# Kernel optimization log

Measured on AMD Instinct MI355X. Metric: run time of the kernel, lower is better.

Reference implementation:

```python
import jax, jax.numpy as jnp
import numpy as np

N = 100000   # nodes
E = 1600000  # edges
G = 256      # graphs
NF = 7       # node features
EF = 3       # edge features (in/out)
UD = 2       # global feature dim
H = 128      # hidden dim
NL = 2       # MetaLayers = n_layers - 1
DOUT = 1


def _lin_init(k, fan_in, fan_out):
    return jax.random.normal(k, (fan_in, fan_out), jnp.float32) / np.sqrt(fan_in)


def _mlp2(h, W1, b1, W2, b2):
    return jax.nn.relu(h @ W1 + b1) @ W2 + b2


def setup_inputs() -> dict:
    key = jax.random.key(0)
    ks = jax.random.split(key, 40)
    x = jax.random.normal(ks[0], (N, NF), jnp.float32)
    edge_index = jax.random.randint(ks[1], (2, E), 0, N, jnp.int64)
    edge_attr = jax.random.normal(ks[2], (E, EF), jnp.float32)
    u = jax.random.normal(ks[3], (G, UD), jnp.float32)
    batch = jnp.sort(jax.random.randint(ks[4], (N,), 0, G, jnp.int64))
    # stacked per-layer params (NL identical layers)
    e_in = 2 * NF + EF          # 17
    n_in = NF + 3 * EF + UD     # 18
    eW1 = jnp.stack([_lin_init(ks[5 + i], e_in, H) for i in range(NL)])
    eb1 = jnp.zeros((NL, H), jnp.float32)
    eW2 = jnp.stack([_lin_init(ks[7 + i], H, EF) for i in range(NL)])
    eb2 = jnp.zeros((NL, EF), jnp.float32)
    nW1 = jnp.stack([_lin_init(ks[9 + i], n_in, H) for i in range(NL)])
    nb1 = jnp.zeros((NL, H), jnp.float32)
    nW2 = jnp.stack([_lin_init(ks[11 + i], H, NF) for i in range(NL)])
    nb2 = jnp.zeros((NL, NF), jnp.float32)
    # output head: 3*node_out + global_in -> H -> H -> H -> dim_out
    oW1 = _lin_init(ks[20], 3 * NF + UD, H); ob1 = jnp.zeros((H,), jnp.float32)
    oW2 = _lin_init(ks[21], H, H); ob2 = jnp.zeros((H,), jnp.float32)
    oW3 = _lin_init(ks[22], H, H); ob3 = jnp.zeros((H,), jnp.float32)
    oW4 = _lin_init(ks[23], H, DOUT); ob4 = jnp.zeros((DOUT,), jnp.float32)
    return dict(x=x, edge_attr=edge_attr, u=u,
                eW1=eW1, eb1=eb1, eW2=eW2, eb2=eb2,
                nW1=nW1, nb1=nb1, nW2=nW2, nb2=nb2,
                oW1=oW1, ob1=ob1, oW2=oW2, ob2=ob2,
                oW3=oW3, ob3=ob3, oW4=oW4, ob4=ob4,
                edge_index=edge_index, batch=batch)


def _segment_reduce3(vals, seg, num):
    # add / max (empty -> 0, matching torch_scatter fill) / mean
    s = jax.ops.segment_sum(vals, seg, num_segments=num)
    cnt = jax.ops.segment_sum(jnp.ones((vals.shape[0], 1), vals.dtype), seg, num_segments=num)
    m = jax.ops.segment_max(vals, seg, num_segments=num)
    m = jnp.where(cnt > 0, m, jnp.zeros_like(m))
    mean = s / jnp.maximum(cnt, 1.0)
    return s, m, mean, cnt


def reference(x, edge_attr, u, eW1, eb1, eW2, eb2, nW1, nb1, nW2, nb2,
              oW1, ob1, oW2, ob2, oW3, ob3, oW4, ob4, edge_index, batch):
    row, col = edge_index[0], edge_index[1]
    for l in range(NL):
        # EdgeModel: gather src/dest node feats + edge feats -> MLP
        e_in = jnp.concatenate([x[row], x[col], edge_attr], axis=1)  # [E, 2*NF+EF]
        edge_attr = _mlp2(e_in, eW1[l], eb1[l], eW2[l], eb2[l])      # [E, EF]
        # NodeModel: three scatter reductions over incoming edges (col)
        s, m, mean, _ = _segment_reduce3(edge_attr, col, N)
        n_in = jnp.concatenate([x, s, m, mean, u[batch]], axis=1)    # [N, NF+3*EF+UD]
        x = _mlp2(n_in, nW1[l], nb1[l], nW2[l], nb2[l])              # [N, NF]
    # global pools per graph
    s, m, mean, _ = _segment_reduce3(x, batch, G)
    h = jnp.concatenate([s, mean, m, u], axis=1)                     # [G, 3*NF+UD]
    h = jax.nn.relu(h @ oW1 + ob1)
    h = jax.nn.relu(h @ oW2 + ob2)
    h = jax.nn.relu(h @ oW3 + ob3)
    return h @ oW4 + ob4                                             # [G, DOUT]
```

## Files before the change

### kernel.cpp

```cpp
#include <hip/hip_runtime.h>

#define NN 100000
#define NE 1600000
#define NG 256
#define NB 391

__global__ __launch_bounds__(256) void zero_kernel(float* __restrict__ p, int n) {
    int i = blockIdx.x * 256 + threadIdx.x;
    if (i < n) p[i] = 0.f;
}

__global__ __launch_bounds__(256) void rank_kernel(
    const int* __restrict__ col, unsigned* __restrict__ cnt,
    unsigned* __restrict__ rank) {
    int e = blockIdx.x * 256 + threadIdx.x;
    rank[e] = atomicAdd(&cnt[col[e]], 1u);
}

__global__ __launch_bounds__(256) void gbound_kernel(
    const int* __restrict__ batch, int* __restrict__ gstart) {
    int n = blockIdx.x * 256 + threadIdx.x;
    if (n >= NN) return;
    int b = batch[n];
    int bp = (n == 0) ? -1 : batch[n - 1];
    for (int g = bp + 1; g <= b; ++g) gstart[g] = n;
    if (n == NN - 1) {
        for (int g = b + 1; g <= NG; ++g) gstart[g] = NN;
    }
}

__global__ __launch_bounds__(256) void bsum_kernel(
    const unsigned* __restrict__ cnt, unsigned* __restrict__ bsum) {
    __shared__ unsigned sm[256];
    int i = blockIdx.x * 256 + threadIdx.x;
    sm[threadIdx.x] = (i < NN) ? cnt[i] : 0u;
    __syncthreads();
    for (int s = 128; s > 0; s >>= 1) {
        if (threadIdx.x < s) sm[threadIdx.x] += sm[threadIdx.x + s];
        __syncthreads();
    }
    if (threadIdx.x == 0) bsum[blockIdx.x] = sm[0];
}

__global__ __launch_bounds__(512) void bscan_kernel(
    const unsigned* __restrict__ bsum, unsigned* __restrict__ boff) {
    __shared__ unsigned a[512], b[512];
    int t = threadIdx.x;
    a[t] = (t < NB) ? bsum[t] : 0u;
    __syncthreads();
    unsigned* src = a; unsigned* dst = b;
    for (int off = 1; off < 512; off <<= 1) {
        unsigned v = src[t];
        if (t >= off) v += src[t - off];
        dst[t] = v;
        __syncthreads();
        unsigned* tmp = src; src = dst; dst = tmp;
    }
    if (t < NB) boff[t] = (t == 0) ? 0u : src[t - 1];
}

__global__ __launch_bounds__(256) void start_kernel(
    const unsigned* __restrict__ cnt, const unsigned* __restrict__ boff,
    unsigned* __restrict__ start) {
    __shared__ unsigned a[256], b[256];
    int t = threadIdx.x;
    int i = blockIdx.x * 256 + t;
    unsigned v = (i < NN) ? cnt[i] : 0u;
    a[t] = v;
    __syncthreads();
    unsigned* src = a; unsigned* dst = b;
    for (int off = 1; off < 256; off <<= 1) {
        unsigned x = src[t];
        if (t >= off) x += src[t - off];
        dst[t] = x;
        __syncthreads();
        unsigned* tmp = src; src = dst; dst = tmp;
    }
    unsigned excl = src[t] - v;
    unsigned st = boff[blockIdx.x] + excl;
    if (i < NN) {
        start[i] = st;
        if (i == NN - 1) start[NN] = st + v;
    }
}

__global__ __launch_bounds__(256) void scatter_kernel(
    const int* __restrict__ row, const int* __restrict__ col,
    const float* __restrict__ ea,
    const unsigned* __restrict__ start, const unsigned* __restrict__ rank,
    int2* __restrict__ rc, float* __restrict__ eab) {
    int e = blockIdx.x * 256 + threadIdx.x;
    int c = col[e];
    unsigned t = start[c] + rank[e];
    rc[t] = make_int2(row[e], c);
    eab[(size_t)t * 3 + 0] = ea[(size_t)e * 3 + 0];
    eab[(size_t)t * 3 + 1] = ea[(size_t)e * 3 + 1];
    eab[(size_t)t * 3 + 2] = ea[(size_t)e * 3 + 2];
}

__global__ __launch_bounds__(256) void prep_kernel(
    const float* __restrict__ eW1, const float* __restrict__ eb1, const float* __restrict__ eW2,
    const float* __restrict__ nW1, const float* __restrict__ nb1, const float* __restrict__ nW2,
    float* __restrict__ ewt, float* __restrict__ nwt)
{
    int t = blockIdx.x * 256 + threadIdx.x;
    const int ESZ = 2 * 128 * 24;
    const int NSZ = 2 * 128 * 28;
    if (t < ESZ) {
        int l = t / (128 * 24), rest = t % (128 * 24), j = rest / 24, i = rest % 24;
        float v = 0.f;
        if (i < 17)       v = eW1[l * 17 * 128 + i * 128 + j];
        else if (i == 17) v = eb1[l * 128 + j];
        else if (i < 21)  v = eW2[l * 128 * 3 + j * 3 + (i - 18)];
        ewt[t] = v;
    } else if (t < ESZ + NSZ) {
        int q = t - ESZ;
        int l = q / (128 * 28), rest = q % (128 * 28), j = rest / 28, i = rest % 28;
        float v = 0.f;
        if (i < 18)       v = nW1[l * 18 * 128 + i * 128 + j];
        else if (i == 18) v = nb1[l * 128 + j];
        else if (i < 26)  v = nW2[l * 128 * 7 + j * 7 + (i - 19)];
        nwt[q] = v;
    }
}

__global__ __launch_bounds__(256) void edge_kernel(
    const float* __restrict__ x, float* eab,
    const int2* __restrict__ rc,
    const float* __restrict__ wt, const float* __restrict__ b2)
{
    int base = blockIdx.x * 1024 + threadIdx.x;
    int tt[4];
    bool ok[4];
    float in[4][17];

    #pragma unroll
    for (int k = 0; k < 4; ++k) {
        int t = base + k * 256;
        ok[k] = (t < NE);
        tt[k] = ok[k] ? t : 0;
        int2 p = rc[tt[k]];
        const float* xr = x + (size_t)p.x * 7;
        const float* xc = x + (size_t)p.y * 7;
        #pragma unroll
        for (int i = 0; i < 7; ++i) in[k][i] = xr[i];
        #pragma unroll
        for (int i = 0; i < 7; ++i) in[k][7 + i] = xc[i];
        #pragma unroll
        for (int i = 0; i < 3; ++i) in[k][14 + i] = eab[(size_t)tt[k] * 3 + i];
    }

    asm volatile("" : "+v"(in[0][0]), "+v"(in[0][1]), "+v"(in[0][2]), "+v"(in[0][3]),
                      "+v"(in[0][4]), "+v"(in[0][5]), "+v"(in[0][6]), "+v"(in[0][7]),
                      "+v"(in[0][8]), "+v"(in[0][9]), "+v"(in[0][10]), "+v"(in[0][11]),
                      "+v"(in[0][12]), "+v"(in[0][13]), "+v"(in[0][14]), "+v"(in[0][15]),
                      "+v"(in[0][16]));
    asm volatile("" : "+v"(in[1][0]), "+v"(in[1][1]), "+v"(in[1][2]), "+v"(in[1][3]),
                      "+v"(in[1][4]), "+v"(in[1][5]), "+v"(in[1][6]), "+v"(in[1][7]),
                      "+v"(in[1][8]), "+v"(in[1][9]), "+v"(in[1][10]), "+v"(in[1][11]),
                      "+v"(in[1][12]), "+v"(in[1][13]), "+v"(in[1][14]), "+v"(in[1][15]),
                      "+v"(in[1][16]));
    asm volatile("" : "+v"(in[2][0]), "+v"(in[2][1]), "+v"(in[2][2]), "+v"(in[2][3]),
                      "+v"(in[2][4]), "+v"(in[2][5]), "+v"(in[2][6]), "+v"(in[2][7]),
                      "+v"(in[2][8]), "+v"(in[2][9]), "+v"(in[2][10]), "+v"(in[2][11]),
                      "+v"(in[2][12]), "+v"(in[2][13]), "+v"(in[2][14]), "+v"(in[2][15]),
                      "+v"(in[2][16]));
    asm volatile("" : "+v"(in[3][0]), "+v"(in[3][1]), "+v"(in[3][2]), "+v"(in[3][3]),
                      "+v"(in[3][4]), "+v"(in[3][5]), "+v"(in[3][6]), "+v"(in[3][7]),
                      "+v"(in[3][8]), "+v"(in[3][9]), "+v"(in[3][10]), "+v"(in[3][11]),
                      "+v"(in[3][12]), "+v"(in[3][13]), "+v"(in[3][14]), "+v"(in[3][15]),
                      "+v"(in[3][16]));

    float acc[4][3];
    #pragma unroll
    for (int k = 0; k < 4; ++k) { acc[k][0] = 0.f; acc[k][1] = 0.f; acc[k][2] = 0.f; }

    #pragma unroll 4
    for (int j = 0; j < 128; ++j) {
        const float* wr = wt + __builtin_amdgcn_readfirstlane(j * 24);
        float w[21];
        #pragma unroll
        for (int i = 0; i < 21; ++i) w[i] = wr[i];
        float h0[4], h1[4];
        #pragma unroll
        for (int k = 0; k < 4; ++k) { h0[k] = w[17]; h1[k] = 0.f; }
        #pragma unroll
        for (int k = 0; k < 4; ++k) {
            h0[k] += in[k][0] * w[0];   h1[k] += in[k][1] * w[1];
            h0[k] += in[k][2] * w[2];   h1[k] += in[k][3] * w[3];
            h0[k] += in[k][4] * w[4];   h1[k] += in[k][5] * w[5];
            h0[k] += in[k][6] * w[6];   h1[k] += in[k][7] * w[7];
            h0[k] += in[k][8] * w[8];   h1[k] += in[k][9] * w[9];
            h0[k] += in[k][10] * w[10]; h1[k] += in[k][11] * w[11];
            h0[k] += in[k][12] * w[12]; h1[k] += in[k][13] * w[13];
            h0[k] += in[k][14] * w[14]; h1[k] += in[k][15] * w[15];
            h0[k] += in[k][16] * w[16];
        }
        #pragma unroll
        for (int k = 0; k < 4; ++k) {
            float h = fmaxf(h0[k] + h1[k], 0.f);
            acc[k][0] += h * w[18];
            acc[k][1] += h * w[19];
            acc[k][2] += h * w[20];
        }
    }

    float bb0 = b2[0], bb1 = b2[1], bb2 = b2[2];
    #pragma unroll
    for (int k = 0; k < 4; ++k) {
        if (ok[k]) {
            eab[(size_t)tt[k] * 3 + 0] = acc[k][0] + bb0;
            eab[(size_t)tt[k] * 3 + 1] = acc[k][1] + bb1;
            eab[(size_t)tt[k] * 3 + 2] = acc[k][2] + bb2;
        }
    }
}

__global__ __launch_bounds__(256) void reduce_kernel(
    const float* __restrict__ eab, const unsigned* __restrict__ start,
    const float* __restrict__ u, const int* __restrict__ batch,
    float* __restrict__ nred)
{
    int gid = blockIdx.x * 256 + threadIdx.x;
    int n = gid >> 4, sub = gid & 15;
    if (n >= NN) return;
    unsigned sbeg = start[n], send = start[n + 1];

    float s0 = 0.f, s1 = 0.f, s2 = 0.f;
    float m0 = -__builtin_inff(), m1 = -__builtin_inff(), m2 = -__builtin_inff();
    for (unsigned k = sbeg + sub; k < send; k += 16) {
        float v0 = eab[(size_t)k * 3 + 0];
        float v1 = eab[(size_t)k * 3 + 1];
        float v2 = eab[(size_t)k * 3 + 2];
        s0 += v0; s1 += v1; s2 += v2;
        m0 = fmaxf(m0, v0); m1 = fmaxf(m1, v1); m2 = fmaxf(m2, v2);
    }
    #pragma unroll
    for (int msk = 1; msk < 16; msk <<= 1) {
        s0 += __shfl_xor(s0, msk, 16);
        s1 += __shfl_xor(s1, msk, 16);
        s2 += __shfl_xor(s2, msk, 16);
        m0 = fmaxf(m0, __shfl_xor(m0, msk, 16));
        m1 = fmaxf(m1, __shfl_xor(m1, msk, 16));
        m2 = fmaxf(m2, __shfl_xor(m2, msk, 16));
    }
    if (sub == 0) {
        float deg = (float)(send - sbeg);
        if (send == sbeg) { m0 = 0.f; m1 = 0.f; m2 = 0.f; }
        float inv = 1.f / fmaxf(deg, 1.f);
        int b = batch[n];
        float* o = nred + (size_t)n * 12;
        o[0] = s0; o[1] = s1; o[2] = s2;
        o[3] = m0; o[4] = m1; o[5] = m2;
        o[6] = s0 * inv; o[7] = s1 * inv; o[8] = s2 * inv;
        o[9] = u[b * 2 + 0]; o[10] = u[b * 2 + 1];
    }
}

#define NMLP_BLOCKS 1024
#define NMLP_WAVES (NMLP_BLOCKS * 4)
__global__ __launch_bounds__(256, 4) void nodemlp_kernel(
    const float* x_in, const float* __restrict__ nred,
    const float* __restrict__ wt, const float* __restrict__ b2,
    float* x_out)
{
    int lane = threadIdx.x & 63;
    int wid = (blockIdx.x * 256 + threadIdx.x) >> 6;

    const float* ra = wt + lane * 28;
    const float* rb = wt + (lane + 64) * 28;
    float a0 = ra[0], a1 = ra[1], a2 = ra[2], a3 = ra[3], a4 = ra[4], a5 = ra[5],
          a6 = ra[6], a7 = ra[7], a8 = ra[8], a9 = ra[9], a10 = ra[10], a11 = ra[11],
          a12 = ra[12], a13 = ra[13], a14 = ra[14], a15 = ra[15], a16 = ra[16], a17 = ra[17],
          ab = ra[18], p0 = ra[19], p1 = ra[20], p2 = ra[21], p3 = ra[22], p4 = ra[23],
          p5 = ra[24], p6 = ra[25];
    float b0 = rb[0], b1 = rb[1], b2_ = rb[2], b3 = rb[3], b4 = rb[4], b5 = rb[5],
          b6 = rb[6], b7 = rb[7], b8 = rb[8], b9 = rb[9], b10 = rb[10], b11 = rb[11],
          b12 = rb[12], b13 = rb[13], b14 = rb[14], b15 = rb[15], b16 = rb[16], b17 = rb[17],
          bb = rb[18], q0 = rb[19], q1 = rb[20], q2 = rb[21], q3 = rb[22], q4 = rb[23],
          q5 = rb[24], q6 = rb[25];

    asm volatile("" : "+v"(a0), "+v"(a1), "+v"(a2), "+v"(a3), "+v"(a4), "+v"(a5),
                      "+v"(a6), "+v"(a7), "+v"(a8), "+v"(a9), "+v"(a10), "+v"(a11),
                      "+v"(a12), "+v"(a13), "+v"(a14), "+v"(a15), "+v"(a16), "+v"(a17),
                      "+v"(ab), "+v"(p0), "+v"(p1), "+v"(p2), "+v"(p3), "+v"(p4),
                      "+v"(p5), "+v"(p6));
    asm volatile("" : "+v"(b0), "+v"(b1), "+v"(b2_), "+v"(b3), "+v"(b4), "+v"(b5),
                      "+v"(b6), "+v"(b7), "+v"(b8), "+v"(b9), "+v"(b10), "+v"(b11),
                      "+v"(b12), "+v"(b13), "+v"(b14), "+v"(b15), "+v"(b16), "+v"(b17),
                      "+v"(bb), "+v"(q0), "+v"(q1), "+v"(q2), "+v"(q3), "+v"(q4),
                      "+v"(q5), "+v"(q6));

    float B0 = b2[0], B1 = b2[1], B2 = b2[2], B3 = b2[3], B4 = b2[4], B5 = b2[5], B6 = b2[6];

    const int nper = (NN + NMLP_WAVES - 1) / NMLP_WAVES;
    int n0 = wid * nper;
    int n1 = n0 + nper; if (n1 > NN) n1 = NN;

    #pragma unroll 2
    for (int n = n0; n < n1; ++n) {
        int nu = __builtin_amdgcn_readfirstlane(n);
        const float* xp = x_in + (size_t)nu * 7;
        const float* rp = nred + (size_t)nu * 12;
        float i0 = xp[0], i1 = xp[1], i2 = xp[2], i3 = xp[3], i4 = xp[4], i5 = xp[5], i6 = xp[6];
        float s0 = rp[0], s1 = rp[1], s2 = rp[2];
        float m0 = rp[3], m1 = rp[4], m2 = rp[5];
        float e0 = rp[6], e1 = rp[7], e2 = rp[8];
        float u0 = rp[9], u1 = rp[10];

        float ha = ab, hb = bb;
        ha += i0 * a0;  hb += i0 * b0;
        ha += i1 * a1;  hb += i1 * b1;
        ha += i2 * a2;  hb += i2 * b2_;
        ha += i3 * a3;  hb += i3 * b3;
        ha += i4 * a4;  hb += i4 * b4;
        ha += i5 * a5;  hb += i5 * b5;
        ha += i6 * a6;  hb += i6 * b6;
        ha += s0 * a7;  hb += s0 * b7;
        ha += s1 * a8;  hb += s1 * b8;
        ha += s2 * a9;  hb += s2 * b9;
        ha += m0 * a10; hb += m0 * b10;
        ha += m1 * a11; hb += m1 * b11;
        ha += m2 * a12; hb += m2 * b12;
        ha += e0 * a13; hb += e0 * b13;
        ha += e1 * a14; hb += e1 * b14;
        ha += e2 * a15; hb += e2 * b15;
        ha += u0 * a16; hb += u0 * b16;
        ha += u1 * a17; hb += u1 * b17;
        ha = fmaxf(ha, 0.f); hb = fmaxf(hb, 0.f);

        float c0 = ha * p0 + hb * q0;
        float c1 = ha * p1 + hb * q1;
        float c2 = ha * p2 + hb * q2;
        float c3 = ha * p3 + hb * q3;
        float c4 = ha * p4 + hb * q4;
        float c5 = ha * p5 + hb * q5;
        float c6 = ha * p6 + hb * q6;
        #pragma unroll
        for (int msk = 1; msk < 64; msk <<= 1) {
            c0 += __shfl_xor(c0, msk);
            c1 += __shfl_xor(c1, msk);
            c2 += __shfl_xor(c2, msk);
            c3 += __shfl_xor(c3, msk);
            c4 += __shfl_xor(c4, msk);
            c5 += __shfl_xor(c5, msk);
            c6 += __shfl_xor(c6, msk);
        }
        float o = c0 + B0;
        if (lane == 1) o = c1 + B1;
        if (lane == 2) o = c2 + B2;
        if (lane == 3) o = c3 + B3;
        if (lane == 4) o = c4 + B4;
        if (lane == 5) o = c5 + B5;
        if (lane == 6) o = c6 + B6;
        if (lane < 7) x_out[(size_t)nu * 7 + lane] = o;
    }
}

__global__ __launch_bounds__(256) void pool_head_kernel(
    const float* __restrict__ x, const int* __restrict__ gstart,
    const float* __restrict__ u,
    const float* __restrict__ oW1, const float* __restrict__ ob1,
    const float* __restrict__ oW2, const float* __restrict__ ob2,
    const float* __restrict__ oW3, const float* __restrict__ ob3,
    const float* __restrict__ oW4, const float* __restrict__ ob4,
    float* __restrict__ out)
{
    int g = blockIdx.x, tid = threadIdx.x;
    int lane = tid & 63, wv = tid >> 6;
    int gs = gstart[g], ge = gstart[g + 1];

    float s0 = 0.f, s1 = 0.f, s2 = 0.f, s3 = 0.f, s4 = 0.f, s5 = 0.f, s6 = 0.f;
    float m0 = -__builtin_inff(), m1 = m0, m2 = m0, m3 = m0, m4 = m0, m5 = m0, m6 = m0;
    for (int n = gs + tid; n < ge; n += 256) {
        const float* xp = x + (size_t)n * 7;
        float v0 = xp[0], v1 = xp[1], v2 = xp[2], v3 = xp[3], v4 = xp[4], v5 = xp[5], v6 = xp[6];
        s0 += v0; s1 += v1; s2 += v2; s3 += v3; s4 += v4; s5 += v5; s6 += v6;
        m0 = fmaxf(m0, v0); m1 = fmaxf(m1, v1); m2 = fmaxf(m2, v2); m3 = fmaxf(m3, v3);
        m4 = fmaxf(m4, v4); m5 = fmaxf(m5, v5); m6 = fmaxf(m6, v6);
    }
    #pragma unroll
    for (int msk = 1; msk < 64; msk <<= 1) {
        s0 += __shfl_xor(s0, msk); s1 += __shfl_xor(s1, msk); s2 += __shfl_xor(s2, msk);
        s3 += __shfl_xor(s3, msk); s4 += __shfl_xor(s4, msk); s5 += __shfl_xor(s5, msk);
        s6 += __shfl_xor(s6, msk);
        m0 = fmaxf(m0, __shfl_xor(m0, msk)); m1 = fmaxf(m1, __shfl_xor(m1, msk));
        m2 = fmaxf(m2, __shfl_xor(m2, msk)); m3 = fmaxf(m3, __shfl_xor(m3, msk));
        m4 = fmaxf(m4, __shfl_xor(m4, msk)); m5 = fmaxf(m5, __shfl_xor(m5, msk));
        m6 = fmaxf(m6, __shfl_xor(m6, msk));
    }
    __shared__ float red[4][14];
    __shared__ float hin[23];
    __shared__ float ha[128];
    __shared__ float hbuf[128];
    if (lane == 0) {
        red[wv][0] = s0; red[wv][1] = s1; red[wv][2] = s2; red[wv][3] = s3;
        red[wv][4] = s4; red[wv][5] = s5; red[wv][6] = s6;
        red[wv][7] = m0; red[wv][8] = m1; red[wv][9] = m2; red[wv][10] = m3;
        red[wv][11] = m4; red[wv][12] = m5; red[wv][13] = m6;
    }
    __syncthreads();
    if (tid < 7) {
        float S = red[0][tid] + red[1][tid] + red[2][tid] + red[3][tid];
        float M = fmaxf(fmaxf(red[0][7 + tid], red[1][7 + tid]),
                        fmaxf(red[2][7 + tid], red[3][7 + tid]));
        float cntf = (float)(ge - gs);
        if (ge == gs) M = 0.f;
        hin[tid] = S;
        hin[7 + tid] = S / fmaxf(cntf, 1.f);
        hin[14 + tid] = M;
    }
    if (tid < 2) hin[21 + tid] = u[g * 2 + tid];
    __syncthreads();

    float h = 0.f;
    if (tid < 128) {
        h = ob1[tid];
        for (int i = 0; i < 23; ++i) h += hin[i] * oW1[i * 128 + tid];
        ha[tid] = fmaxf(h, 0.f);
    }
    __syncthreads();
    if (tid < 128) {
        h = ob2[tid];
        for (int i = 0; i < 128; ++i) h += ha[i] * oW2[i * 128 + tid];
        hbuf[tid] = fmaxf(h, 0.f);
    }
    __syncthreads();
    if (tid < 128) {
        h = ob3[tid];
        for (int i = 0; i < 128; ++i) h += hbuf[i] * oW3[i * 128 + tid];
        ha[tid] = fmaxf(h, 0.f) * oW4[tid];
    }
    __syncthreads();
    if (tid == 0) {
        float acc = ob4[0];
        for (int i = 0; i < 128; ++i) acc += ha[i];
        out[g] = acc;
    }
}

extern "C" void kernel_launch(void* const* d_in, const int* in_sizes, int n_in,
                              void* d_out, int out_size, void* d_ws, size_t ws_size,
                              hipStream_t stream) {
    const float* x         = (const float*)d_in[0];
    const float* edge_attr = (const float*)d_in[1];
    const float* u         = (const float*)d_in[2];
    const float* eW1 = (const float*)d_in[3];
    const float* eb1 = (const float*)d_in[4];
    const float* eW2 = (const float*)d_in[5];
    const float* eb2 = (const float*)d_in[6];
    const float* nW1 = (const float*)d_in[7];
    const float* nb1 = (const float*)d_in[8];
    const float* nW2 = (const float*)d_in[9];
    const float* nb2 = (const float*)d_in[10];
    const float* oW1 = (const float*)d_in[11];
    const float* ob1 = (const float*)d_in[12];
    const float* oW2 = (const float*)d_in[13];
    const float* ob2 = (const float*)d_in[14];
    const float* oW3 = (const float*)d_in[15];
    const float* ob3 = (const float*)d_in[16];
    const float* oW4 = (const float*)d_in[17];
    const float* ob4 = (const float*)d_in[18];
    const int* edge_index = (const int*)d_in[19];
    const int* batch      = (const int*)d_in[20];
    const int* row = edge_index;
    const int* col = edge_index + NE;

    float* ws        = (float*)d_ws;
    float* eab       = ws;
    float* ws_x      = eab + (size_t)NE * 3;
    int2*  rc        = (int2*)(ws_x + (size_t)NN * 7);
    float* nred      = (float*)(rc + (size_t)NE);
    unsigned* rank   = (unsigned*)(nred + (size_t)NN * 12);
    unsigned* cnt    = rank + (size_t)NE;
    unsigned* startv = cnt + NN;
    unsigned* bsum   = startv + NN + 1;
    unsigned* boff   = bsum + 512;
    int* gstart      = (int*)(boff + 512);
    float* ewt       = (float*)(gstart + 260);
    float* nwt       = ewt + 2 * 128 * 24;

    dim3 b256(256);
    dim3 ge_(NE / 256);
    dim3 ge4((NE + 1023) / 1024);
    dim3 gn(NB);

    zero_kernel<<<(NN + 255) / 256, b256, 0, stream>>>((float*)cnt, NN);

    rank_kernel<<<ge_, b256, 0, stream>>>(col, cnt, rank);
    gbound_kernel<<<gn, b256, 0, stream>>>(batch, gstart);
    bsum_kernel<<<gn, b256, 0, stream>>>(cnt, bsum);
    bscan_kernel<<<1, 512, 0, stream>>>(bsum, boff);
    start_kernel<<<gn, b256, 0, stream>>>(cnt, boff, startv);
    scatter_kernel<<<ge_, b256, 0, stream>>>(row, col, edge_attr, startv, rank, rc, eab);

    {
        int t = 2 * 128 * 24 + 2 * 128 * 28;
        prep_kernel<<<(t + 255) / 256, b256, 0, stream>>>(eW1, eb1, eW2, nW1, nb1, nW2, ewt, nwt);
    }

    dim3 gr((NN * 16 + 255) / 256);

    edge_kernel<<<ge4, b256, 0, stream>>>(x, eab, rc, ewt, eb2);
    reduce_kernel<<<gr, b256, 0, stream>>>(eab, startv, u, batch, nred);
    nodemlp_kernel<<<NMLP_BLOCKS, b256, 0, stream>>>(x, nred, nwt, nb2, ws_x);

    edge_kernel<<<ge4, b256, 0, stream>>>(ws_x, eab, rc, ewt + 128 * 24, eb2 + 3);
    reduce_kernel<<<gr, b256, 0, stream>>>(eab, startv, u, batch, nred);
    nodemlp_kernel<<<NMLP_BLOCKS, b256, 0, stream>>>(ws_x, nred, nwt + 128 * 28, nb2 + 7, ws_x);

    pool_head_kernel<<<NG, b256, 0, stream>>>(ws_x, gstart, u,
        oW1, ob1, oW2, ob2, oW3, ob3, oW4, ob4, (float*)d_out);
}
```

Baseline: 479.7 us.

## Compute edge MLP first layer with bf16 MFMA instead of scalar FMAs

The edge MLP's first layer (17->128) now runs on matrix cores via 16x16x32 bf16 MFMA. Inputs and weights are packed to bf16, and the edge kernel becomes a grid-stride loop over 16-edge tiles per wave. The second layer (128->3) is done per lane with a cross-lane shuffle reduction, and prep_kernel lays the weights out in MFMA fragment order. This removes a large scalar FMA load but gives up precision by rounding the inputs and first-layer weights to bf16.

```diff
diff --git a/kernel.cpp b/kernel.cpp
--- a/kernel.cpp
+++ b/kernel.cpp
@@ -4,6 +4,14 @@
 #define NE 1600000
 #define NG 256
 #define NB 391
+
+typedef __attribute__((ext_vector_type(8))) short short8v;
+typedef __attribute__((ext_vector_type(4))) float float4v;
+
+__device__ __forceinline__ unsigned short f2bf(float f) {
+    unsigned u = __float_as_uint(f);
+    return (unsigned short)((u + 0x7FFFu + ((u >> 16) & 1u)) >> 16);
+}
 
 __global__ __launch_bounds__(256) void zero_kernel(float* __restrict__ p, int n) {
     int i = blockIdx.x * 256 + threadIdx.x;
@@ -101,20 +109,36 @@
 __global__ __launch_bounds__(256) void prep_kernel(
     const float* __restrict__ eW1, const float* __restrict__ eb1, const float* __restrict__ eW2,
     const float* __restrict__ nW1, const float* __restrict__ nb1, const float* __restrict__ nW2,
-    float* __restrict__ ewt, float* __restrict__ nwt)
+    short* __restrict__ ewf, float* __restrict__ w2f, float* __restrict__ b1f,
+    float* __restrict__ nwt)
 {
     int t = blockIdx.x * 256 + threadIdx.x;
-    const int ESZ = 2 * 128 * 24;
-    const int NSZ = 2 * 128 * 28;
-    if (t < ESZ) {
-        int l = t / (128 * 24), rest = t % (128 * 24), j = rest / 24, i = rest % 24;
-        float v = 0.f;
-        if (i < 17)       v = eW1[l * 17 * 128 + i * 128 + j];
-        else if (i == 17) v = eb1[l * 128 + j];
-        else if (i < 21)  v = eW2[l * 128 * 3 + j * 3 + (i - 18)];
-        ewt[t] = v;
-    } else if (t < ESZ + NSZ) {
-        int q = t - ESZ;
+    const int EWF = 2 * 4096;
+    const int W2F = 2 * 1536;
+    const int B1F = 2 * 512;
+    const int NWT = 2 * 128 * 28;
+    if (t < EWF) {
+        int layer = t >> 12, r = t & 4095;
+        int tt = r >> 9, r2 = r & 511;
+        int l = r2 >> 3, i = r2 & 7;
+        int kk = ((l >> 4) << 3) + i;
+        int n = tt * 16 + (l & 15);
+        float v = (kk < 17) ? eW1[layer * 17 * 128 + kk * 128 + n] : 0.f;
+        ewf[t] = (short)f2bf(v);
+    } else if (t < EWF + W2F) {
+        int q = t - EWF;
+        int layer = q / 1536, r = q % 1536;
+        int l = r / 24, r2 = r % 24;
+        int tt = r2 / 3, c = r2 % 3;
+        int k = tt * 16 + (l & 15);
+        w2f[q] = eW2[layer * 384 + k * 3 + c];
+    } else if (t < EWF + W2F + B1F) {
+        int q = t - EWF - W2F;
+        int layer = q / 512, r = q % 512;
+        int l = r / 8, tt = r % 8;
+        b1f[q] = eb1[layer * 128 + tt * 16 + (l & 15)];
+    } else if (t < EWF + W2F + B1F + NWT) {
+        int q = t - EWF - W2F - B1F;
         int l = q / (128 * 28), rest = q % (128 * 28), j = rest / 28, i = rest % 28;
         float v = 0.f;
         if (i < 18)       v = nW1[l * 18 * 128 + i * 128 + j];
@@ -127,91 +151,90 @@
 __global__ __launch_bounds__(256) void edge_kernel(
     const float* __restrict__ x, float* eab,
     const int2* __restrict__ rc,
-    const float* __restrict__ wt, const float* __restrict__ b2)
+    const short* __restrict__ ewf, const float* __restrict__ w2f,
+    const float* __restrict__ b1f, const float* __restrict__ b2)
 {
-    int base = blockIdx.x * 1024 + threadIdx.x;
-    int tt[4];
-    bool ok[4];
-    float in[4][17];
-
+    int lane = threadIdx.x & 63;
+    int l15 = lane & 15, lg = lane >> 4;
+    int wid = (blockIdx.x * 256 + threadIdx.x) >> 6;
+    int nwaves = gridDim.x * 4;
+
+    short8v B1[8];
     #pragma unroll
-    for (int k = 0; k < 4; ++k) {
-        int t = base + k * 256;
-        ok[k] = (t < NE);
-        tt[k] = ok[k] ? t : 0;
-        int2 p = rc[tt[k]];
+    for (int t = 0; t < 8; ++t)
+        B1[t] = *(const short8v*)(ewf + (t * 64 + lane) * 8);
+    float w2a[8], w2b[8], w2c[8], b1v[8];
+    #pragma unroll
+    for (int t = 0; t < 8; ++t) {
+        w2a[t] = w2f[lane * 24 + t * 3 + 0];
+        w2b[t] = w2f[lane * 24 + t * 3 + 1];
+        w2c[t] = w2f[lane * 24 + t * 3 + 2];
+        b1v[t] = b1f[lane * 8 + t];
+    }
+    float bb0 = b2[0], bb1 = b2[1], bb2 = b2[2];
+
+    const int NT = NE / 16;
+    for (int tile = wid; tile < NT; tile += nwaves) {
+        int s = tile * 16 + l15;
+        int2 p = rc[s];
         const float* xr = x + (size_t)p.x * 7;
         const float* xc = x + (size_t)p.y * 7;
+        const float* ep = eab + (size_t)s * 3;
+
+        float av0 = 0.f, av1 = 0.f, av2 = 0.f, av3 = 0.f,
+              av4 = 0.f, av5 = 0.f, av6 = 0.f, av7 = 0.f;
+        if (lg == 0) {
+            av0 = xr[0]; av1 = xr[1]; av2 = xr[2]; av3 = xr[3];
+            av4 = xr[4]; av5 = xr[5]; av6 = xr[6]; av7 = xc[0];
+        } else if (lg == 1) {
+            av0 = xc[1]; av1 = xc[2]; av2 = xc[3]; av3 = xc[4];
+            av4 = xc[5]; av5 = xc[6]; av6 = ep[0]; av7 = ep[1];
+        } else if (lg == 2) {
+            av0 = ep[2];
+        }
+
+        short8v A;
+        A[0] = (short)f2bf(av0); A[1] = (short)f2bf(av1);
+        A[2] = (short)f2bf(av2); A[3] = (short)f2bf(av3);
+        A[4] = (short)f2bf(av4); A[5] = (short)f2bf(av5);
+        A[6] = (short)f2bf(av6); A[7] = (short)f2bf(av7);
+
+        float4v Z = {0.f, 0.f, 0.f, 0.f};
+        float4v C[8];
         #pragma unroll
-        for (int i = 0; i < 7; ++i) in[k][i] = xr[i];
+        for (int t = 0; t < 8; ++t)
+            C[t] = __builtin_amdgcn_mfma_f32_16x16x32_bf16(A, B1[t], Z, 0, 0, 0);
+
+        float p00 = 0.f, p01 = 0.f, p02 = 0.f;
+        float p10 = 0.f, p11 = 0.f, p12 = 0.f;
+        float p20 = 0.f, p21 = 0.f, p22 = 0.f;
+        float p30 = 0.f, p31 = 0.f, p32 = 0.f;
         #pragma unroll
-        for (int i = 0; i < 7; ++i) in[k][7 + i] = xc[i];
-        #pragma unroll
-        for (int i = 0; i < 3; ++i) in[k][14 + i] = eab[(size_t)tt[k] * 3 + i];
-    }
-
-    asm volatile("" : "+v"(in[0][0]), "+v"(in[0][1]), "+v"(in[0][2]), "+v"(in[0][3]),
-                      "+v"(in[0][4]), "+v"(in[0][5]), "+v"(in[0][6]), "+v"(in[0][7]),
-                      "+v"(in[0][8]), "+v"(in[0][9]), "+v"(in[0][10]), "+v"(in[0][11]),
-                      "+v"(in[0][12]), "+v"(in[0][13]), "+v"(in[0][14]), "+v"(in[0][15]),
-                      "+v"(in[0][16]));
-    asm volatile("" : "+v"(in[1][0]), "+v"(in[1][1]), "+v"(in[1][2]), "+v"(in[1][3]),
-                      "+v"(in[1][4]), "+v"(in[1][5]), "+v"(in[1][6]), "+v"(in[1][7]),
-                      "+v"(in[1][8]), "+v"(in[1][9]), "+v"(in[1][10]), "+v"(in[1][11]),
-                      "+v"(in[1][12]), "+v"(in[1][13]), "+v"(in[1][14]), "+v"(in[1][15]),
-                      "+v"(in[1][16]));
-    asm volatile("" : "+v"(in[2][0]), "+v"(in[2][1]), "+v"(in[2][2]), "+v"(in[2][3]),
-                      "+v"(in[2][4]), "+v"(in[2][5]), "+v"(in[2][6]), "+v"(in[2][7]),
-                      "+v"(in[2][8]), "+v"(in[2][9]), "+v"(in[2][10]), "+v"(in[2][11]),
-                      "+v"(in[2][12]), "+v"(in[2][13]), "+v"(in[2][14]), "+v"(in[2][15]),
-                      "+v"(in[2][16]));
-    asm volatile("" : "+v"(in[3][0]), "+v"(in[3][1]), "+v"(in[3][2]), "+v"(in[3][3]),
-                      "+v"(in[3][4]), "+v"(in[3][5]), "+v"(in[3][6]), "+v"(in[3][7]),
-                      "+v"(in[3][8]), "+v"(in[3][9]), "+v"(in[3][10]), "+v"(in[3][11]),
-                      "+v"(in[3][12]), "+v"(in[3][13]), "+v"(in[3][14]), "+v"(in[3][15]),
-                      "+v"(in[3][16]));
-
-    float acc[4][3];
-    #pragma unroll
-    for (int k = 0; k < 4; ++k) { acc[k][0] = 0.f; acc[k][1] = 0.f; acc[k][2] = 0.f; }
-
-    #pragma unroll 4
-    for (int j = 0; j < 128; ++j) {
-        const float* wr = wt + __builtin_amdgcn_readfirstlane(j * 24);
-        float w[21];
-        #pragma unroll
-        for (int i = 0; i < 21; ++i) w[i] = wr[i];
-        float h0[4], h1[4];
-        #pragma unroll
-        for (int k = 0; k < 4; ++k) { h0[k] = w[17]; h1[k] = 0.f; }
-        #pragma unroll
-        for (int k = 0; k < 4; ++k) {
-            h0[k] += in[k][0] * w[0];   h1[k] += in[k][1] * w[1];
-            h0[k] += in[k][2] * w[2];   h1[k] += in[k][3] * w[3];
-            h0[k] += in[k][4] * w[4];   h1[k] += in[k][5] * w[5];
-            h0[k] += in[k][6] * w[6];   h1[k] += in[k][7] * w[7];
-            h0[k] += in[k][8] * w[8];   h1[k] += in[k][9] * w[9];
-            h0[k] += in[k][10] * w[10]; h1[k] += in[k][11] * w[11];
-            h0[k] += in[k][12] * w[12]; h1[k] += in[k][13] * w[13];
-            h0[k] += in[k][14] * w[14]; h1[k] += in[k][15] * w[15];
-            h0[k] += in[k][16] * w[16];
+        for (int t = 0; t < 8; ++t) {
+            float h0 = fmaxf(C[t][0] + b1v[t], 0.f);
+            float h1 = fmaxf(C[t][1] + b1v[t], 0.f);
+            float h2 = fmaxf(C[t][2] + b1v[t], 0.f);
+            float h3 = fmaxf(C[t][3] + b1v[t], 0.f);
+            p00 += h0 * w2a[t]; p01 += h0 * w2b[t]; p02 += h0 * w2c[t];
+            p10 += h1 * w2a[t]; p11 += h1 * w2b[t]; p12 += h1 * w2c[t];
+            p20 += h2 * w2a[t]; p21 += h2 * w2b[t]; p22 += h2 * w2c[t];
+            p30 += h3 * w2a[t]; p31 += h3 * w2b[t]; p32 += h3 * w2c[t];
         }
         #pragma unroll
-        for (int k = 0; k < 4; ++k) {
-            float h = fmaxf(h0[k] + h1[k], 0.f);
-            acc[k][0] += h * w[18];
-            acc[k][1] += h * w[19];
-            acc[k][2] += h * w[20];
+        for (int m = 1; m < 16; m <<= 1) {
+            p00 += __shfl_xor(p00, m, 16); p01 += __shfl_xor(p01, m, 16); p02 += __shfl_xor(p02, m, 16);
+            p10 += __shfl_xor(p10, m, 16); p11 += __shfl_xor(p11, m, 16); p12 += __shfl_xor(p12, m, 16);
+            p20 += __shfl_xor(p20, m, 16); p21 += __shfl_xor(p21, m, 16); p22 += __shfl_xor(p22, m, 16);
+            p30 += __shfl_xor(p30, m, 16); p31 += __shfl_xor(p31, m, 16); p32 += __shfl_xor(p32, m, 16);
         }
-    }
-
-    float bb0 = b2[0], bb1 = b2[1], bb2 = b2[2];
-    #pragma unroll
-    for (int k = 0; k < 4; ++k) {
-        if (ok[k]) {
-            eab[(size_t)tt[k] * 3 + 0] = acc[k][0] + bb0;
-            eab[(size_t)tt[k] * 3 + 1] = acc[k][1] + bb1;
-            eab[(size_t)tt[k] * 3 + 2] = acc[k][2] + bb2;
+        if (l15 < 4) {
+            float o0 = (l15 == 0) ? p00 : (l15 == 1) ? p10 : (l15 == 2) ? p20 : p30;
+            float o1 = (l15 == 0) ? p01 : (l15 == 1) ? p11 : (l15 == 2) ? p21 : p31;
+            float o2 = (l15 == 0) ? p02 : (l15 == 1) ? p12 : (l15 == 2) ? p22 : p32;
+            size_t off = (size_t)(tile * 16 + lg * 4 + l15) * 3;
+            eab[off + 0] = o0 + bb0;
+            eab[off + 1] = o1 + bb1;
+            eab[off + 2] = o2 + bb2;
         }
     }
 }
@@ -477,12 +500,14 @@
     unsigned* bsum   = startv + NN + 1;
     unsigned* boff   = bsum + 512;
     int* gstart      = (int*)(boff + 512);
-    float* ewt       = (float*)(gstart + 260);
-    float* nwt       = ewt + 2 * 128 * 24;
+    float* nwt       = (float*)(gstart + 260);
+    float* w2f       = nwt + 2 * 128 * 28;
+    float* b1f       = w2f + 2 * 1536;
+    uintptr_t ewb    = ((uintptr_t)(b1f + 2 * 512) + 15) & ~(uintptr_t)15;
+    short* ewf       = (short*)ewb;
 
     dim3 b256(256);
     dim3 ge_(NE / 256);
-    dim3 ge4((NE + 1023) / 1024);
     dim3 gn(NB);
 
     zero_kernel<<<(NN + 255) / 256, b256, 0, stream>>>((float*)cnt, NN);
@@ -495,17 +520,20 @@
     scatter_kernel<<<ge_, b256, 0, stream>>>(row, col, edge_attr, startv, rank, rc, eab);
 
     {
-        int t = 2 * 128 * 24 + 2 * 128 * 28;
-        prep_kernel<<<(t + 255) / 256, b256, 0, stream>>>(eW1, eb1, eW2, nW1, nb1, nW2, ewt, nwt);
+        int t = 2 * 4096 + 2 * 1536 + 2 * 512 + 2 * 128 * 28;
+        prep_kernel<<<(t + 255) / 256, b256, 0, stream>>>(
+            eW1, eb1, eW2, nW1, nb1, nW2, ewf, w2f, b1f, nwt);
     }
 
     dim3 gr((NN * 16 + 255) / 256);
-
-    edge_kernel<<<ge4, b256, 0, stream>>>(x, eab, rc, ewt, eb2);
+    dim3 gemf(2048);
+
+    edge_kernel<<<gemf, b256, 0, stream>>>(x, eab, rc, ewf, w2f, b1f, eb2);
     reduce_kernel<<<gr, b256, 0, stream>>>(eab, startv, u, batch, nred);
     nodemlp_kernel<<<NMLP_BLOCKS, b256, 0, stream>>>(x, nred, nwt, nb2, ws_x);
 
-    edge_kernel<<<ge4, b256, 0, stream>>>(ws_x, eab, rc, ewt + 128 * 24, eb2 + 3);
+    edge_kernel<<<gemf, b256, 0, stream>>>(ws_x, eab, rc,
+        ewf + 4096, w2f + 1536, b1f + 512, eb2 + 3);
     reduce_kernel<<<gr, b256, 0, stream>>>(eab, startv, u, batch, nred);
     nodemlp_kernel<<<NMLP_BLOCKS, b256, 0, stream>>>(ws_x, nred, nwt + 128 * 28, nb2 + 7, ws_x);
 
```

Result: faster. 427.0 us (-11.0%).
